# Optimization experiments

Measured on AMD Instinct MI355X. Metric: run time of the kernel, lower is better.

The kernel has to match this reference:

```python
import jax, jax.numpy as jnp
import numpy as np

SORB = 64      # spin orbitals (sequence length)
NELE = 32      # electrons
H = 512        # num_hiddens
B = 4096       # batch
ALPHA = NELE // 2                      # = beta = 16 (spin-up / spin-down electrons)
MIN_I = min(SORB - 2 * ALPHA, 2 * ALPHA)  # = 32; symmetry mask active for i >= MIN_I
EPS = 1e-12


def setup_inputs() -> dict:
    key = jax.random.key(0)
    ks = jax.random.split(key, 10)
    s_in = 1.0 / np.sqrt(2.0)
    s_h = 1.0 / np.sqrt(H)
    return {
        "x": jax.random.randint(ks[0], (B, SORB), 0, 2, dtype=jnp.int32),  # occupancies {0,1}
        "W_ih0": jax.random.normal(ks[1], (3 * H, 2), jnp.float32) * s_in,   # GRU layer0 input weights (r,z,n)
        "W_hh0": jax.random.normal(ks[2], (3 * H, H), jnp.float32) * s_h,
        "W_ih1": jax.random.normal(ks[3], (3 * H, H), jnp.float32) * s_h,    # GRU layer1
        "W_hh1": jax.random.normal(ks[4], (3 * H, H), jnp.float32) * s_h,
        "W_amp": jax.random.normal(ks[5], (2, H), jnp.float32) * s_h,
        "b_amp": jax.random.normal(ks[6], (2,), jnp.float32) * 0.01,
        "W_phase": jax.random.normal(ks[7], (2, H), jnp.float32) * s_h,
        "b_phase": jax.random.normal(ks[8], (2,), jnp.float32) * 0.01,
    }


def _gru_cell(x_in, h, Wih, Whh):
    # PyTorch GRU (bias=False), gate order r, z, n
    gi = x_in @ Wih.T          # (B, 3H)
    gh = h @ Whh.T             # (B, 3H)
    r = jax.nn.sigmoid(gi[:, :H] + gh[:, :H])
    z = jax.nn.sigmoid(gi[:, H:2 * H] + gh[:, H:2 * H])
    n = jnp.tanh(gi[:, 2 * H:] + r * gh[:, 2 * H:])
    return (1.0 - z) * n + z * h


def reference(x, W_ih0, W_hh0, W_ih1, W_hh1, W_amp, b_amp, W_phase, b_phase):
    dt = W_ih0.dtype
    bits = x.astype(jnp.int32)           # (B, SORB) occupancies
    nb = bits.shape[0]

    def step(carry, inp):
        h0, h1, x0, amp, phase, nup, ndn = carry
        i, b_i = inp                      # site index, occupancy bits (B,)
        h0n = _gru_cell(x0, h0, W_ih0, W_hh0)
        h1n = _gru_cell(h0n, h1, W_ih1, W_hh1)
        y = h1n                           # (B, H)
        # amplitude: sqrt(softmax(linear))
        y_amp = jnp.sqrt(jax.nn.softmax(y @ W_amp.T + b_amp, axis=1))   # (B, 2)
        # phase: pi * softsign(linear)
        ph = y @ W_phase.T + b_phase
        y_ph = jnp.pi * ph / (1.0 + jnp.abs(ph))
        # particle-number symmetry mask (alpha == beta spin sectors)
        is_even = (i % 2) == 0            # even sites: spin-up, odd: spin-down
        cnt = jnp.where(is_even, nup, ndn)
        lower = (ALPHA - SORB // 2 + i // 2).astype(dt)
        occ_ok = (cnt < ALPHA).astype(dt)
        unocc_ok = (cnt > lower).astype(dt)
        mask = jnp.stack([unocc_ok, occ_ok], axis=1)
        masked = y_amp * mask
        masked = masked / jnp.sqrt(jnp.sum(masked * masked, axis=1, keepdims=True) + EPS)
        y_amp = jnp.where(i >= MIN_I, masked, y_amp)
        # accumulate conditional amplitude / phase at the sampled occupancy
        sel_a = jnp.take_along_axis(y_amp, b_i[:, None], axis=1)[:, 0]
        sel_p = jnp.take_along_axis(y_ph, b_i[:, None], axis=1)[:, 0]
        amp = amp * sel_a
        phase = phase + sel_p
        bf = b_i.astype(dt)
        nup = nup + jnp.where(is_even, bf, 0.0)
        ndn = ndn + jnp.where(is_even, 0.0, bf)
        x0n = jax.nn.one_hot(b_i, 2, dtype=dt)  # next-step GRU input
        return (h0n, h1n, x0n, amp, phase, nup, ndn), None

    init = (
        jnp.zeros((nb, H), dt), jnp.zeros((nb, H), dt), jnp.zeros((nb, 2), dt),
        jnp.ones((nb,), dt), jnp.zeros((nb,), dt), jnp.zeros((nb,), dt), jnp.zeros((nb,), dt),
    )
    xs = (jnp.arange(SORB), bits.T)       # scan over sites
    (_, _, _, amp, phase, _, _), _ = jax.lax.scan(step, init, xs)
    # complex wavefunction psi = amp * exp(1j*phase); returned as real pair (amp, phase)
    return jnp.stack([amp, phase], axis=-1)
```

## Files before the change

### kernel.cpp

```cpp
#include <hip/hip_runtime.h>
#include <hip/hip_bf16.h>

#define SORB  64
#define HID   512
#define BATCH 4096
#define N3H   1536
#define KD    512
#define BK    64
#define PI_F  3.14159265358979f

typedef _Float16 half8 __attribute__((ext_vector_type(8)));
typedef float    floatx4 __attribute__((ext_vector_type(4)));

__device__ __forceinline__ void gload16(const void* g, void* l) {
    __builtin_amdgcn_global_load_lds(
        (const __attribute__((address_space(1))) void*)g,
        (__attribute__((address_space(3))) void*)l, 16, 0, 0);
}

__device__ __forceinline__ float sigmoidf_(float x) { return 1.f / (1.f + __expf(-x)); }
__device__ __forceinline__ float tanhf_(float x) {
    x = fminf(fmaxf(x, -15.f), 15.f);
    const float e2 = __expf(2.f * x);
    return (e2 - 1.f) / (e2 + 1.f);
}

__global__ __launch_bounds__(256) void convw_kernel(
    const float* __restrict__ w0, const float* __restrict__ w1, const float* __restrict__ w2,
    _Float16* __restrict__ o0, _Float16* __restrict__ o1, _Float16* __restrict__ o2)
{
    const int i = blockIdx.x * 256 + threadIdx.x;
    if (i < N3H * KD) {
        o0[i] = (_Float16)w0[i];
        o1[i] = (_Float16)w1[i];
        o2[i] = (_Float16)w2[i];
    }
}

__global__ __launch_bounds__(256) void init_kernel(
    float* __restrict__ amp, float* __restrict__ phase,
    int* __restrict__ nup, int* __restrict__ ndn)
{
    const int i = blockIdx.x * 256 + threadIdx.x;
    if (i < BATCH) { amp[i] = 1.f; phase[i] = 0.f; nup[i] = 0; ndn[i] = 0; }
}

__device__ __forceinline__ void head_row(
    const _Float16* __restrict__ h1, int m,
    const float* __restrict__ Wamp, const float* __restrict__ bamp,
    const float* __restrict__ Wph,  const float* __restrict__ bph,
    const int* __restrict__ bits,
    float* __restrict__ amp, float* __restrict__ phase,
    int* __restrict__ nup, int* __restrict__ ndn,
    float* __restrict__ out, int step, int lane)
{
    const half8 hv = *(const half8*)(h1 + (size_t)m * HID + lane * 8);
    float d0 = 0.f, d1 = 0.f, d2 = 0.f, d3 = 0.f;
#pragma unroll
    for (int e = 0; e < 8; ++e) {
        const int j = lane * 8 + e;
        const float hn = (float)hv[e];
        d0 += hn * Wamp[j];       d1 += hn * Wamp[HID + j];
        d2 += hn * Wph[j];        d3 += hn * Wph[HID + j];
    }
#pragma unroll
    for (int off = 1; off < 64; off <<= 1) {
        d0 += __shfl_xor(d0, off); d1 += __shfl_xor(d1, off);
        d2 += __shfl_xor(d2, off); d3 += __shfl_xor(d3, off);
    }
    if (lane == 0) {
        const float a0 = d0 + bamp[0];
        const float a1 = d1 + bamp[1];
        const float mx = fmaxf(a0, a1);
        const float e0 = __expf(a0 - mx), e1 = __expf(a1 - mx);
        const float inv = 1.f / (e0 + e1);
        float ya0 = sqrtf(e0 * inv), ya1 = sqrtf(e1 * inv);
        const float p0 = d2 + bph[0];
        const float p1 = d3 + bph[1];
        const float yp0 = PI_F * p0 / (1.f + fabsf(p0));
        const float yp1 = PI_F * p1 / (1.f + fabsf(p1));
        const int even = ((step & 1) == 0);
        const int cnt = even ? nup[m] : ndn[m];
        if (step >= 32) {
            const int lower = (step >> 1) - 16;
            const float m0v = (cnt > lower) ? ya0 : 0.f;
            const float m1v = (cnt < 16) ? ya1 : 0.f;
            const float nrm = sqrtf(m0v * m0v + m1v * m1v + 1e-12f);
            ya0 = m0v / nrm; ya1 = m1v / nrm;
        }
        const int bi = bits[m * SORB + step];
        const float na = amp[m] * (bi ? ya1 : ya0);
        const float np = phase[m] + (bi ? yp1 : yp0);
        amp[m] = na; phase[m] = np;
        if (bi) { if (even) nup[m] = cnt + 1; else ndn[m] = cnt + 1; }
        if (step == SORB - 1) {
            out[m * 2 + 0] = na;
            out[m * 2 + 1] = np;
        }
    }
}

__global__ __launch_bounds__(256) void step1_kernel(
    const _Float16* __restrict__ h0h_c, const _Float16* __restrict__ h1h_c,
    const _Float16* __restrict__ wh0,   const _Float16* __restrict__ wh1,
    const float* __restrict__ Wih0, const int* __restrict__ bits,
    float* __restrict__ h0f, _Float16* __restrict__ h0h_n,
    _Float16* __restrict__ gB, int step,
    const float* __restrict__ Wamp, const float* __restrict__ bamp,
    const float* __restrict__ Wph,  const float* __restrict__ bph,
    float* __restrict__ amp, float* __restrict__ phase,
    int* __restrict__ nup, int* __restrict__ ndn, float* __restrict__ out)
{
    const int z = blockIdx.z;
    const _Float16* Aop = z ? h1h_c : h0h_c;
    const _Float16* Wop = z ? wh1 : wh0;
    const int j0 = blockIdx.x * 64;
    const int m0 = blockIdx.y * 64;

    __shared__ __align__(16) _Float16 As[64 * BK];
    __shared__ __align__(16) _Float16 Bs[192 * BK];

    const int tid  = threadIdx.x;
    const int lane = tid & 63;
    const int wid  = tid >> 6;
    const int wm   = wid >> 1, wj = wid & 1;
    const int ku   = lane >> 4;

    floatx4 acc[2][2][3];
    const floatx4 z4 = {0.f, 0.f, 0.f, 0.f};
#pragma unroll
    for (int a = 0; a < 2; ++a)
#pragma unroll
        for (int b = 0; b < 2; ++b)
#pragma unroll
            for (int g = 0; g < 3; ++g) acc[a][b][g] = z4;

    const _Float16* a_srcp[2];
#pragma unroll
    for (int k2 = 0; k2 < 2; ++k2) {
        const int p = tid + k2 * 256, row = p >> 3, c = (p & 7) ^ (row & 7);
        a_srcp[k2] = Aop + (size_t)(m0 + row) * KD + c * 8;
    }
    const _Float16* b_srcp[6];
#pragma unroll
    for (int k2 = 0; k2 < 6; ++k2) {
        const int p = tid + k2 * 256, row = p >> 3, c = (p & 7) ^ (row & 7);
        const int grow = (row >> 6) * HID + j0 + (row & 63);
        b_srcp[k2] = Wop + (size_t)grow * KD + c * 8;
    }
    _Float16* a_dst[2];
#pragma unroll
    for (int k2 = 0; k2 < 2; ++k2) a_dst[k2] = As + (size_t)(k2 * 256 + wid * 64) * 8;
    _Float16* b_dst[6];
#pragma unroll
    for (int k2 = 0; k2 < 6; ++k2) b_dst[k2] = Bs + (size_t)(k2 * 256 + wid * 64) * 8;

    int aoff[2][2], boff[2][3][2];
#pragma unroll
    for (int mf = 0; mf < 2; ++mf) {
        const int r = wm * 32 + mf * 16 + (lane & 15);
#pragma unroll
        for (int kk = 0; kk < 2; ++kk)
            aoff[mf][kk] = r * BK + (((kk * 4 + ku) ^ (r & 7)) * 8);
    }
#pragma unroll
    for (int jf = 0; jf < 2; ++jf)
#pragma unroll
        for (int g = 0; g < 3; ++g) {
            const int r = g * 64 + wj * 32 + jf * 16 + (lane & 15);
#pragma unroll
            for (int kk = 0; kk < 2; ++kk)
                boff[jf][g][kk] = r * BK + (((kk * 4 + ku) ^ (r & 7)) * 8);
        }

    for (int kt = 0; kt < 8; ++kt) {
        const int k0 = kt * BK;
#pragma unroll
        for (int k2 = 0; k2 < 2; ++k2) gload16(a_srcp[k2] + k0, a_dst[k2]);
#pragma unroll
        for (int k2 = 0; k2 < 6; ++k2) gload16(b_srcp[k2] + k0, b_dst[k2]);
        __syncthreads();
#pragma unroll
        for (int kk = 0; kk < 2; ++kk) {
            half8 af[2], bf[2][3];
#pragma unroll
            for (int mf = 0; mf < 2; ++mf) af[mf] = *(const half8*)(As + aoff[mf][kk]);
#pragma unroll
            for (int jf = 0; jf < 2; ++jf)
#pragma unroll
                for (int g = 0; g < 3; ++g) bf[jf][g] = *(const half8*)(Bs + boff[jf][g][kk]);
#pragma unroll
            for (int mf = 0; mf < 2; ++mf)
#pragma unroll
                for (int jf = 0; jf < 2; ++jf)
#pragma unroll
                    for (int g = 0; g < 3; ++g)
                        acc[mf][jf][g] = __builtin_amdgcn_mfma_f32_16x16x32_f16(
                            af[mf], bf[jf][g], acc[mf][jf][g], 0, 0, 0);
        }
        __syncthreads();
    }

    if (z == 0) {
#pragma unroll
        for (int mf = 0; mf < 2; ++mf)
#pragma unroll
            for (int jf = 0; jf < 2; ++jf) {
                const floatx4 gr = acc[mf][jf][0];
                const floatx4 gz = acc[mf][jf][1];
                const floatx4 gn = acc[mf][jf][2];
#pragma unroll
                for (int reg = 0; reg < 4; ++reg) {
                    const int m = m0 + wm * 32 + mf * 16 + (lane >> 4) * 4 + reg;
                    const int j = j0 + wj * 32 + jf * 16 + (lane & 15);
                    float gir = 0.f, giz = 0.f, gin = 0.f;
                    if (step > 0) {
                        const int tb = bits[m * SORB + step - 1];
                        gir = Wih0[j * 2 + tb];
                        giz = Wih0[(HID + j) * 2 + tb];
                        gin = Wih0[(2 * HID + j) * 2 + tb];
                    }
                    const float r  = sigmoidf_(gir + gr[reg]);
                    const float zz = sigmoidf_(giz + gz[reg]);
                    const float n  = tanhf_(gin + r * gn[reg]);
                    const size_t idx = (size_t)m * HID + j;
                    const float h  = h0f[idx];
                    const float hn = (1.f - zz) * n + zz * h;
                    h0f[idx]   = hn;
                    h0h_n[idx] = (_Float16)hn;
                }
            }
    } else {
#pragma unroll
        for (int mf = 0; mf < 2; ++mf)
#pragma unroll
            for (int jf = 0; jf < 2; ++jf)
#pragma unroll
                for (int g = 0; g < 3; ++g)
#pragma unroll
                    for (int reg = 0; reg < 4; ++reg) {
                        const int m = m0 + wm * 32 + mf * 16 + (lane >> 4) * 4 + reg;
                        const int j = j0 + wj * 32 + jf * 16 + (lane & 15);
                        gB[(size_t)m * N3H + g * HID + j] = (_Float16)acc[mf][jf][g][reg];
                    }
        if (step > 0) {
            const int t = blockIdx.y * 8 + blockIdx.x;
#pragma unroll
            for (int rr = 0; rr < 2; ++rr) {
                const int m = t * 8 + wid * 2 + rr;
                head_row(h1h_c, m, Wamp, bamp, Wph, bph, bits,
                         amp, phase, nup, ndn, out, step - 1, lane);
            }
        }
    }
}

__global__ __launch_bounds__(256) void step2_kernel(
    const _Float16* __restrict__ h0h_n, const _Float16* __restrict__ wi1,
    const _Float16* __restrict__ gB,
    float* __restrict__ h1f, _Float16* __restrict__ h1h_n)
{
    const int j0 = blockIdx.x * 64;
    const int m0 = blockIdx.y * 64;

    __shared__ __align__(16) _Float16 As[64 * BK];
    __shared__ __align__(16) _Float16 Bs[192 * BK];

    const int tid  = threadIdx.x;
    const int lane = tid & 63;
    const int wid  = tid >> 6;
    const int wm   = wid >> 1, wj = wid & 1;
    const int ku   = lane >> 4;

    floatx4 acc[2][2][3];
    const floatx4 z4 = {0.f, 0.f, 0.f, 0.f};
#pragma unroll
    for (int a = 0; a < 2; ++a)
#pragma unroll
        for (int b = 0; b < 2; ++b)
#pragma unroll
            for (int g = 0; g < 3; ++g) acc[a][b][g] = z4;

    const _Float16* a_srcp[2];
#pragma unroll
    for (int k2 = 0; k2 < 2; ++k2) {
        const int p = tid + k2 * 256, row = p >> 3, c = (p & 7) ^ (row & 7);
        a_srcp[k2] = h0h_n + (size_t)(m0 + row) * KD + c * 8;
    }
    const _Float16* b_srcp[6];
#pragma unroll
    for (int k2 = 0; k2 < 6; ++k2) {
        const int p = tid + k2 * 256, row = p >> 3, c = (p & 7) ^ (row & 7);
        const int grow = (row >> 6) * HID + j0 + (row & 63);
        b_srcp[k2] = wi1 + (size_t)grow * KD + c * 8;
    }
    _Float16* a_dst[2];
#pragma unroll
    for (int k2 = 0; k2 < 2; ++k2) a_dst[k2] = As + (size_t)(k2 * 256 + wid * 64) * 8;
    _Float16* b_dst[6];
#pragma unroll
    for (int k2 = 0; k2 < 6; ++k2) b_dst[k2] = Bs + (size_t)(k2 * 256 + wid * 64) * 8;

    int aoff[2][2], boff[2][3][2];
#pragma unroll
    for (int mf = 0; mf < 2; ++mf) {
        const int r = wm * 32 + mf * 16 + (lane & 15);
#pragma unroll
        for (int kk = 0; kk < 2; ++kk)
            aoff[mf][kk] = r * BK + (((kk * 4 + ku) ^ (r & 7)) * 8);
    }
#pragma unroll
    for (int jf = 0; jf < 2; ++jf)
#pragma unroll
        for (int g = 0; g < 3; ++g) {
            const int r = g * 64 + wj * 32 + jf * 16 + (lane & 15);
#pragma unroll
            for (int kk = 0; kk < 2; ++kk)
                boff[jf][g][kk] = r * BK + (((kk * 4 + ku) ^ (r & 7)) * 8);
        }

    for (int kt = 0; kt < 8; ++kt) {
        const int k0 = kt * BK;
#pragma unroll
        for (int k2 = 0; k2 < 2; ++k2) gload16(a_srcp[k2] + k0, a_dst[k2]);
#pragma unroll
        for (int k2 = 0; k2 < 6; ++k2) gload16(b_srcp[k2] + k0, b_dst[k2]);
        __syncthreads();
#pragma unroll
        for (int kk = 0; kk < 2; ++kk) {
            half8 af[2], bf[2][3];
#pragma unroll
            for (int mf = 0; mf < 2; ++mf) af[mf] = *(const half8*)(As + aoff[mf][kk]);
#pragma unroll
            for (int jf = 0; jf < 2; ++jf)
#pragma unroll
                for (int g = 0; g < 3; ++g) bf[jf][g] = *(const half8*)(Bs + boff[jf][g][kk]);
#pragma unroll
            for (int mf = 0; mf < 2; ++mf)
#pragma unroll
                for (int jf = 0; jf < 2; ++jf)
#pragma unroll
                    for (int g = 0; g < 3; ++g)
                        acc[mf][jf][g] = __builtin_amdgcn_mfma_f32_16x16x32_f16(
                            af[mf], bf[jf][g], acc[mf][jf][g], 0, 0, 0);
        }
        __syncthreads();
    }

#pragma unroll
    for (int mf = 0; mf < 2; ++mf)
#pragma unroll
        for (int jf = 0; jf < 2; ++jf) {
            const floatx4 gr = acc[mf][jf][0];
            const floatx4 gz = acc[mf][jf][1];
            const floatx4 gn = acc[mf][jf][2];
#pragma unroll
            for (int reg = 0; reg < 4; ++reg) {
                const int m = m0 + wm * 32 + mf * 16 + (lane >> 4) * 4 + reg;
                const int j = j0 + wj * 32 + jf * 16 + (lane & 15);
                const size_t gbase = (size_t)m * N3H;
                const float ghr = (float)gB[gbase + j];
                const float ghz = (float)gB[gbase + HID + j];
                const float ghn = (float)gB[gbase + 2 * HID + j];
                const float r  = sigmoidf_(gr[reg] + ghr);
                const float zz = sigmoidf_(gz[reg] + ghz);
                const float n  = tanhf_(gn[reg] + r * ghn);
                const size_t idx = (size_t)m * HID + j;
                const float h  = h1f[idx];
                const float hn = (1.f - zz) * n + zz * h;
                h1f[idx]   = hn;
                h1h_n[idx] = (_Float16)hn;
            }
        }
}

__global__ __launch_bounds__(256) void head_kernel(
    const _Float16* __restrict__ h1h_n,
    const float* __restrict__ Wamp, const float* __restrict__ bamp,
    const float* __restrict__ Wph,  const float* __restrict__ bph,
    const int* __restrict__ bits,
    float* __restrict__ amp, float* __restrict__ phase,
    int* __restrict__ nup, int* __restrict__ ndn,
    float* __restrict__ out, int step)
{
    const int lane = threadIdx.x & 63;
    const int m    = blockIdx.x * 4 + (threadIdx.x >> 6);
    head_row(h1h_n, m, Wamp, bamp, Wph, bph, bits, amp, phase, nup, ndn, out, step, lane);
}

extern "C" void kernel_launch(void* const* d_in, const int* in_sizes, int n_in,
                              void* d_out, int out_size, void* d_ws, size_t ws_size,
                              hipStream_t stream) {
    const int*   bits = (const int*)d_in[0];
    const float* Wih0 = (const float*)d_in[1];
    const float* Whh0 = (const float*)d_in[2];
    const float* Wih1 = (const float*)d_in[3];
    const float* Whh1 = (const float*)d_in[4];
    const float* Wamp = (const float*)d_in[5];
    const float* bamp = (const float*)d_in[6];
    const float* Wph  = (const float*)d_in[7];
    const float* bph  = (const float*)d_in[8];
    float* out = (float*)d_out;

    char* ws = (char*)d_ws;
    size_t off = 0;
    auto alloc = [&](size_t bytes) {
        void* p = ws + off;
        off = (off + bytes + 255) & ~(size_t)255;
        return p;
    };
    _Float16* wh0 = (_Float16*)alloc((size_t)N3H * KD * 2);
    _Float16* wi1 = (_Float16*)alloc((size_t)N3H * KD * 2);
    _Float16* wh1 = (_Float16*)alloc((size_t)N3H * KD * 2);
    float*    h0f = (float*)alloc((size_t)BATCH * HID * 4);
    float*    h1f = (float*)alloc((size_t)BATCH * HID * 4);
    _Float16* h0hA = (_Float16*)alloc((size_t)BATCH * HID * 2);
    _Float16* h0hB = (_Float16*)alloc((size_t)BATCH * HID * 2);
    _Float16* h1hA = (_Float16*)alloc((size_t)BATCH * HID * 2);
    _Float16* h1hB = (_Float16*)alloc((size_t)BATCH * HID * 2);
    _Float16* gB  = (_Float16*)alloc((size_t)BATCH * N3H * 2);
    float*    amp   = (float*)alloc((size_t)BATCH * 4);
    float*    phase = (float*)alloc((size_t)BATCH * 4);
    int*      nup   = (int*)alloc((size_t)BATCH * 4);
    int*      ndn   = (int*)alloc((size_t)BATCH * 4);

    _Float16* h0h[2] = {h0hA, h0hB};
    _Float16* h1h[2] = {h1hA, h1hB};

    hipMemsetAsync(h0f, 0, (size_t)BATCH * HID * 4, stream);
    hipMemsetAsync(h1f, 0, (size_t)BATCH * HID * 4, stream);
    hipMemsetAsync(h0hA, 0, (size_t)BATCH * HID * 2, stream);
    hipMemsetAsync(h1hA, 0, (size_t)BATCH * HID * 2, stream);
    convw_kernel<<<(N3H * KD + 255) / 256, 256, 0, stream>>>(Whh0, Wih1, Whh1, wh0, wi1, wh1);
    init_kernel<<<BATCH / 256, 256, 0, stream>>>(amp, phase, nup, ndn);

    for (int s = 0; s < SORB; ++s) {
        const int cur = s & 1, nxt = cur ^ 1;
        step1_kernel<<<dim3(8, 64, 2), 256, 0, stream>>>(
            h0h[cur], h1h[cur], wh0, wh1, Wih0, bits, h0f, h0h[nxt], gB, s,
            Wamp, bamp, Wph, bph, amp, phase, nup, ndn, out);
        step2_kernel<<<dim3(8, 64), 256, 0, stream>>>(
            h0h[nxt], wi1, gB, h1f, h1h[nxt]);
    }
    head_kernel<<<BATCH / 4, 256, 0, stream>>>(
        h1h[0], Wamp, bamp, Wph, bph, bits, amp, phase, nup, ndn, out, SORB - 1);
}
```

Measured before the change: 3.400 ms.

## Fuse layer-1 input and hidden GEMMs into one kernel, drop fp32 hidden state

Layer 1's two GEMMs (input-to-hidden and hidden-to-hidden) now run in one kernel that accumulates both K halves in registers. A separate accumulator keeps the n-gate hidden term apart. This removes the fp16 gB intermediate buffer and its global round trip. The fp32 hidden-state copies are dropped, so state is carried only in fp16, which risks accuracy drift over 64 steps. The head now runs as its own kernel every step instead of being fused into step1, which adds a third launch per step; an unused step2_kernel stub remains as dead code.

```diff
diff --git a/kernel.cpp b/kernel.cpp
--- a/kernel.cpp
+++ b/kernel.cpp
@@ -45,16 +45,383 @@
     if (i < BATCH) { amp[i] = 1.f; phase[i] = 0.f; nup[i] = 0; ndn[i] = 0; }
 }
 
-__device__ __forceinline__ void head_row(
-    const _Float16* __restrict__ h1, int m,
+__global__ __launch_bounds__(256) void step1_kernel(
+    const _Float16* __restrict__ h0h_c, const _Float16* __restrict__ wh0,
+    const float* __restrict__ Wih0, const int* __restrict__ bits,
+    _Float16* __restrict__ h0h_n, int step)
+{
+    const int j0 = blockIdx.x * 64;
+    const int m0 = blockIdx.y * 64;
+
+    __shared__ __align__(16) _Float16 As[64 * BK];
+    __shared__ __align__(16) _Float16 Bs[192 * BK];
+
+    const int tid  = threadIdx.x;
+    const int lane = tid & 63;
+    const int wid  = tid >> 6;
+    const int wm   = wid >> 1, wj = wid & 1;
+    const int ku   = lane >> 4;
+
+    floatx4 acc[2][2][3];
+    const floatx4 z4 = {0.f, 0.f, 0.f, 0.f};
+#pragma unroll
+    for (int a = 0; a < 2; ++a)
+#pragma unroll
+        for (int b = 0; b < 2; ++b)
+#pragma unroll
+            for (int g = 0; g < 3; ++g) acc[a][b][g] = z4;
+
+    const _Float16* a_srcp[2];
+#pragma unroll
+    for (int k2 = 0; k2 < 2; ++k2) {
+        const int p = tid + k2 * 256, row = p >> 3, c = (p & 7) ^ (row & 7);
+        a_srcp[k2] = h0h_c + (size_t)(m0 + row) * KD + c * 8;
+    }
+    const _Float16* b_srcp[6];
+#pragma unroll
+    for (int k2 = 0; k2 < 6; ++k2) {
+        const int p = tid + k2 * 256, row = p >> 3, c = (p & 7) ^ (row & 7);
+        const int grow = (row >> 6) * HID + j0 + (row & 63);
+        b_srcp[k2] = wh0 + (size_t)grow * KD + c * 8;
+    }
+    _Float16* a_dst[2];
+#pragma unroll
+    for (int k2 = 0; k2 < 2; ++k2) a_dst[k2] = As + (size_t)(k2 * 256 + wid * 64) * 8;
+    _Float16* b_dst[6];
+#pragma unroll
+    for (int k2 = 0; k2 < 6; ++k2) b_dst[k2] = Bs + (size_t)(k2 * 256 + wid * 64) * 8;
+
+    int aoff[2][2], boff[2][3][2];
+#pragma unroll
+    for (int mf = 0; mf < 2; ++mf) {
+        const int r = wm * 32 + mf * 16 + (lane & 15);
+#pragma unroll
+        for (int kk = 0; kk < 2; ++kk)
+            aoff[mf][kk] = r * BK + (((kk * 4 + ku) ^ (r & 7)) * 8);
+    }
+#pragma unroll
+    for (int jf = 0; jf < 2; ++jf)
+#pragma unroll
+        for (int g = 0; g < 3; ++g) {
+            const int r = g * 64 + wj * 32 + jf * 16 + (lane & 15);
+#pragma unroll
+            for (int kk = 0; kk < 2; ++kk)
+                boff[jf][g][kk] = r * BK + (((kk * 4 + ku) ^ (r & 7)) * 8);
+        }
+
+    for (int kt = 0; kt < 8; ++kt) {
+        const int k0 = kt * BK;
+#pragma unroll
+        for (int k2 = 0; k2 < 2; ++k2) gload16(a_srcp[k2] + k0, a_dst[k2]);
+#pragma unroll
+        for (int k2 = 0; k2 < 6; ++k2) gload16(b_srcp[k2] + k0, b_dst[k2]);
+        __syncthreads();
+#pragma unroll
+        for (int kk = 0; kk < 2; ++kk) {
+            half8 af[2], bf[2][3];
+#pragma unroll
+            for (int mf = 0; mf < 2; ++mf) af[mf] = *(const half8*)(As + aoff[mf][kk]);
+#pragma unroll
+            for (int jf = 0; jf < 2; ++jf)
+#pragma unroll
+                for (int g = 0; g < 3; ++g) bf[jf][g] = *(const half8*)(Bs + boff[jf][g][kk]);
+#pragma unroll
+            for (int mf = 0; mf < 2; ++mf)
+#pragma unroll
+                for (int jf = 0; jf < 2; ++jf)
+#pragma unroll
+                    for (int g = 0; g < 3; ++g)
+                        acc[mf][jf][g] = __builtin_amdgcn_mfma_f32_16x16x32_f16(
+                            af[mf], bf[jf][g], acc[mf][jf][g], 0, 0, 0);
+        }
+        __syncthreads();
+    }
+
+#pragma unroll
+    for (int mf = 0; mf < 2; ++mf)
+#pragma unroll
+        for (int jf = 0; jf < 2; ++jf) {
+            const floatx4 gr = acc[mf][jf][0];
+            const floatx4 gz = acc[mf][jf][1];
+            const floatx4 gn = acc[mf][jf][2];
+#pragma unroll
+            for (int reg = 0; reg < 4; ++reg) {
+                const int m = m0 + wm * 32 + mf * 16 + (lane >> 4) * 4 + reg;
+                const int j = j0 + wj * 32 + jf * 16 + (lane & 15);
+                float gir = 0.f, giz = 0.f, gin = 0.f;
+                if (step > 0) {
+                    const int tb = bits[m * SORB + step - 1];
+                    gir = Wih0[j * 2 + tb];
+                    giz = Wih0[(HID + j) * 2 + tb];
+                    gin = Wih0[(2 * HID + j) * 2 + tb];
+                }
+                const float r  = sigmoidf_(gir + gr[reg]);
+                const float zz = sigmoidf_(giz + gz[reg]);
+                const float n  = tanhf_(gin + r * gn[reg]);
+                const size_t idx = (size_t)m * HID + j;
+                const float h  = (float)h0h_c[idx];
+                h0h_n[idx] = (_Float16)((1.f - zz) * n + zz * h);
+            }
+        }
+}
+
+__global__ __launch_bounds__(256) void step2_kernel(
+    const _Float16* __restrict__ h0h_n, const _Float16* __restrict__ h1h_c,
+    const _Float16* __restrict__ wi1,   const _Float16* __restrict__ wh1,
+    _Float16* __restrict__ h1h_n)
+{
+    const int j0 = blockIdx.x * 64;
+    const int m0 = blockIdx.y * 64;
+
+    __shared__ __align__(16) _Float16 As[64 * BK];
+    __shared__ __align__(16) _Float16 Bs[192 * BK];
+
+    const int tid  = threadIdx.x;
+    const int lane = tid & 63;
+    const int wid  = tid >> 6;
+    const int wm   = wid >> 1, wj = wid & 1;
+    const int ku   = lane >> 4;
+
+    floatx4 acc[2][2][3];
+    const floatx4 z4 = {0.f, 0.f, 0.f, 0.f};
+#pragma unroll
+    for (int a = 0; a < 2; ++a)
+#pragma unroll
+        for (int b = 0; b < 2; ++b)
+#pragma unroll
+            for (int g = 0; g < 3; ++g) acc[a][b][g] = z4;
+
+    _Float16* a_dst[2];
+#pragma unroll
+    for (int k2 = 0; k2 < 2; ++k2) a_dst[k2] = As + (size_t)(k2 * 256 + wid * 64) * 8;
+    _Float16* b_dst[6];
+#pragma unroll
+    for (int k2 = 0; k2 < 6; ++k2) b_dst[k2] = Bs + (size_t)(k2 * 256 + wid * 64) * 8;
+
+    int aoff[2][2], boff[2][3][2];
+#pragma unroll
+    for (int mf = 0; mf < 2; ++mf) {
+        const int r = wm * 32 + mf * 16 + (lane & 15);
+#pragma unroll
+        for (int kk = 0; kk < 2; ++kk)
+            aoff[mf][kk] = r * BK + (((kk * 4 + ku) ^ (r & 7)) * 8);
+    }
+#pragma unroll
+    for (int jf = 0; jf < 2; ++jf)
+#pragma unroll
+        for (int g = 0; g < 3; ++g) {
+            const int r = g * 64 + wj * 32 + jf * 16 + (lane & 15);
+#pragma unroll
+            for (int kk = 0; kk < 2; ++kk)
+                boff[jf][g][kk] = r * BK + (((kk * 4 + ku) ^ (r & 7)) * 8);
+        }
+
+#pragma unroll 1
+    for (int half = 0; half < 2; ++half) {
+        const _Float16* Aop = half ? h1h_c : h0h_n;
+        const _Float16* Wop = half ? wh1  : wi1;
+        const _Float16* a_srcp[2];
+#pragma unroll
+        for (int k2 = 0; k2 < 2; ++k2) {
+            const int p = tid + k2 * 256, row = p >> 3, c = (p & 7) ^ (row & 7);
+            a_srcp[k2] = Aop + (size_t)(m0 + row) * KD + c * 8;
+        }
+        const _Float16* b_srcp[6];
+#pragma unroll
+        for (int k2 = 0; k2 < 6; ++k2) {
+            const int p = tid + k2 * 256, row = p >> 3, c = (p & 7) ^ (row & 7);
+            const int grow = (row >> 6) * HID + j0 + (row & 63);
+            b_srcp[k2] = Wop + (size_t)grow * KD + c * 8;
+        }
+
+        for (int kt = 0; kt < 8; ++kt) {
+            const int k0 = kt * BK;
+#pragma unroll
+            for (int k2 = 0; k2 < 2; ++k2) gload16(a_srcp[k2] + k0, a_dst[k2]);
+#pragma unroll
+            for (int k2 = 0; k2 < 6; ++k2) gload16(b_srcp[k2] + k0, b_dst[k2]);
+            __syncthreads();
+#pragma unroll
+            for (int kk = 0; kk < 2; ++kk) {
+                half8 af[2], bf[2][3];
+#pragma unroll
+                for (int mf = 0; mf < 2; ++mf) af[mf] = *(const half8*)(As + aoff[mf][kk]);
+#pragma unroll
+                for (int jf = 0; jf < 2; ++jf)
+#pragma unroll
+                    for (int g = 0; g < 3; ++g) bf[jf][g] = *(const half8*)(Bs + boff[jf][g][kk]);
+#pragma unroll
+                for (int mf = 0; mf < 2; ++mf)
+#pragma unroll
+                    for (int jf = 0; jf < 2; ++jf)
+#pragma unroll
+                        for (int g = 0; g < 3; ++g)
+                            acc[mf][jf][g] = __builtin_amdgcn_mfma_f32_16x16x32_f16(
+                                af[mf], bf[jf][g], acc[mf][jf][g], 0, 0, 0);
+            }
+            __syncthreads();
+        }
+    }
+
+#pragma unroll
+    for (int mf = 0; mf < 2; ++mf)
+#pragma unroll
+        for (int jf = 0; jf < 2; ++jf) {
+            const floatx4 gr = acc[mf][jf][0];
+            const floatx4 gz = acc[mf][jf][1];
+            const floatx4 gn = acc[mf][jf][2];
+#pragma unroll
+            for (int reg = 0; reg < 4; ++reg) {
+                const int m = m0 + wm * 32 + mf * 16 + (lane >> 4) * 4 + reg;
+                const int j = j0 + wj * 32 + jf * 16 + (lane & 15);
+                const float r  = sigmoidf_(gr[reg]);
+                (void)r;
+            }
+        }
+}
+
+__global__ __launch_bounds__(256) void step2b_kernel(
+    const _Float16* __restrict__ h0h_n, const _Float16* __restrict__ h1h_c,
+    const _Float16* __restrict__ wi1,   const _Float16* __restrict__ wh1,
+    _Float16* __restrict__ h1h_n)
+{
+    const int j0 = blockIdx.x * 64;
+    const int m0 = blockIdx.y * 64;
+
+    __shared__ __align__(16) _Float16 As[64 * BK];
+    __shared__ __align__(16) _Float16 Bs[192 * BK];
+
+    const int tid  = threadIdx.x;
+    const int lane = tid & 63;
+    const int wid  = tid >> 6;
+    const int wm   = wid >> 1, wj = wid & 1;
+    const int ku   = lane >> 4;
+
+    floatx4 acc[2][2][3];
+    floatx4 accn[2][2];
+    const floatx4 z4 = {0.f, 0.f, 0.f, 0.f};
+#pragma unroll
+    for (int a = 0; a < 2; ++a)
+#pragma unroll
+        for (int b = 0; b < 2; ++b) {
+#pragma unroll
+            for (int g = 0; g < 3; ++g) acc[a][b][g] = z4;
+            accn[a][b] = z4;
+        }
+
+    _Float16* a_dst[2];
+#pragma unroll
+    for (int k2 = 0; k2 < 2; ++k2) a_dst[k2] = As + (size_t)(k2 * 256 + wid * 64) * 8;
+    _Float16* b_dst[6];
+#pragma unroll
+    for (int k2 = 0; k2 < 6; ++k2) b_dst[k2] = Bs + (size_t)(k2 * 256 + wid * 64) * 8;
+
+    int aoff[2][2], boff[2][3][2];
+#pragma unroll
+    for (int mf = 0; mf < 2; ++mf) {
+        const int r = wm * 32 + mf * 16 + (lane & 15);
+#pragma unroll
+        for (int kk = 0; kk < 2; ++kk)
+            aoff[mf][kk] = r * BK + (((kk * 4 + ku) ^ (r & 7)) * 8);
+    }
+#pragma unroll
+    for (int jf = 0; jf < 2; ++jf)
+#pragma unroll
+        for (int g = 0; g < 3; ++g) {
+            const int r = g * 64 + wj * 32 + jf * 16 + (lane & 15);
+#pragma unroll
+            for (int kk = 0; kk < 2; ++kk)
+                boff[jf][g][kk] = r * BK + (((kk * 4 + ku) ^ (r & 7)) * 8);
+        }
+
+#pragma unroll 1
+    for (int half = 0; half < 2; ++half) {
+        const _Float16* Aop = half ? h1h_c : h0h_n;
+        const _Float16* Wop = half ? wh1  : wi1;
+        const _Float16* a_srcp[2];
+#pragma unroll
+        for (int k2 = 0; k2 < 2; ++k2) {
+            const int p = tid + k2 * 256, row = p >> 3, c = (p & 7) ^ (row & 7);
+            a_srcp[k2] = Aop + (size_t)(m0 + row) * KD + c * 8;
+        }
+        const _Float16* b_srcp[6];
+#pragma unroll
+        for (int k2 = 0; k2 < 6; ++k2) {
+            const int p = tid + k2 * 256, row = p >> 3, c = (p & 7) ^ (row & 7);
+            const int grow = (row >> 6) * HID + j0 + (row & 63);
+            b_srcp[k2] = Wop + (size_t)grow * KD + c * 8;
+        }
+
+        for (int kt = 0; kt < 8; ++kt) {
+            const int k0 = kt * BK;
+#pragma unroll
+            for (int k2 = 0; k2 < 2; ++k2) gload16(a_srcp[k2] + k0, a_dst[k2]);
+#pragma unroll
+            for (int k2 = 0; k2 < 6; ++k2) gload16(b_srcp[k2] + k0, b_dst[k2]);
+            __syncthreads();
+#pragma unroll
+            for (int kk = 0; kk < 2; ++kk) {
+                half8 af[2], bf[2][3];
+#pragma unroll
+                for (int mf = 0; mf < 2; ++mf) af[mf] = *(const half8*)(As + aoff[mf][kk]);
+#pragma unroll
+                for (int jf = 0; jf < 2; ++jf)
+#pragma unroll
+                    for (int g = 0; g < 3; ++g) bf[jf][g] = *(const half8*)(Bs + boff[jf][g][kk]);
+#pragma unroll
+                for (int mf = 0; mf < 2; ++mf)
+#pragma unroll
+                    for (int jf = 0; jf < 2; ++jf) {
+                        acc[mf][jf][0] = __builtin_amdgcn_mfma_f32_16x16x32_f16(
+                            af[mf], bf[jf][0], acc[mf][jf][0], 0, 0, 0);
+                        acc[mf][jf][1] = __builtin_amdgcn_mfma_f32_16x16x32_f16(
+                            af[mf], bf[jf][1], acc[mf][jf][1], 0, 0, 0);
+                        if (half == 0)
+                            acc[mf][jf][2] = __builtin_amdgcn_mfma_f32_16x16x32_f16(
+                                af[mf], bf[jf][2], acc[mf][jf][2], 0, 0, 0);
+                        else
+                            accn[mf][jf] = __builtin_amdgcn_mfma_f32_16x16x32_f16(
+                                af[mf], bf[jf][2], accn[mf][jf], 0, 0, 0);
+                    }
+            }
+            __syncthreads();
+        }
+    }
+
+#pragma unroll
+    for (int mf = 0; mf < 2; ++mf)
+#pragma unroll
+        for (int jf = 0; jf < 2; ++jf) {
+            const floatx4 grz = acc[mf][jf][0];
+            const floatx4 gzz = acc[mf][jf][1];
+            const floatx4 gin = acc[mf][jf][2];
+            const floatx4 ghn = accn[mf][jf];
+#pragma unroll
+            for (int reg = 0; reg < 4; ++reg) {
+                const int m = m0 + wm * 32 + mf * 16 + (lane >> 4) * 4 + reg;
+                const int j = j0 + wj * 32 + jf * 16 + (lane & 15);
+                const float r  = sigmoidf_(grz[reg]);
+                const float zz = sigmoidf_(gzz[reg]);
+                const float n  = tanhf_(gin[reg] + r * ghn[reg]);
+                const size_t idx = (size_t)m * HID + j;
+                const float h  = (float)h1h_c[idx];
+                h1h_n[idx] = (_Float16)((1.f - zz) * n + zz * h);
+            }
+        }
+}
+
+__global__ __launch_bounds__(256) void head_kernel(
+    const _Float16* __restrict__ h1h_n,
     const float* __restrict__ Wamp, const float* __restrict__ bamp,
     const float* __restrict__ Wph,  const float* __restrict__ bph,
     const int* __restrict__ bits,
     float* __restrict__ amp, float* __restrict__ phase,
     int* __restrict__ nup, int* __restrict__ ndn,
-    float* __restrict__ out, int step, int lane)
+    float* __restrict__ out, int step)
 {
-    const half8 hv = *(const half8*)(h1 + (size_t)m * HID + lane * 8);
+    const int lane = threadIdx.x & 63;
+    const int m    = blockIdx.x * 4 + (threadIdx.x >> 6);
+    const half8 hv = *(const half8*)(h1h_n + (size_t)m * HID + lane * 8);
     float d0 = 0.f, d1 = 0.f, d2 = 0.f, d3 = 0.f;
 #pragma unroll
     for (int e = 0; e < 8; ++e) {
@@ -100,294 +467,6 @@
     }
 }
 
-__global__ __launch_bounds__(256) void step1_kernel(
-    const _Float16* __restrict__ h0h_c, const _Float16* __restrict__ h1h_c,
-    const _Float16* __restrict__ wh0,   const _Float16* __restrict__ wh1,
-    const float* __restrict__ Wih0, const int* __restrict__ bits,
-    float* __restrict__ h0f, _Float16* __restrict__ h0h_n,
-    _Float16* __restrict__ gB, int step,
-    const float* __restrict__ Wamp, const float* __restrict__ bamp,
-    const float* __restrict__ Wph,  const float* __restrict__ bph,
-    float* __restrict__ amp, float* __restrict__ phase,
-    int* __restrict__ nup, int* __restrict__ ndn, float* __restrict__ out)
-{
-    const int z = blockIdx.z;
-    const _Float16* Aop = z ? h1h_c : h0h_c;
-    const _Float16* Wop = z ? wh1 : wh0;
-    const int j0 = blockIdx.x * 64;
-    const int m0 = blockIdx.y * 64;
-
-    __shared__ __align__(16) _Float16 As[64 * BK];
-    __shared__ __align__(16) _Float16 Bs[192 * BK];
-
-    const int tid  = threadIdx.x;
-    const int lane = tid & 63;
-    const int wid  = tid >> 6;
-    const int wm   = wid >> 1, wj = wid & 1;
-    const int ku   = lane >> 4;
-
-    floatx4 acc[2][2][3];
-    const floatx4 z4 = {0.f, 0.f, 0.f, 0.f};
-#pragma unroll
-    for (int a = 0; a < 2; ++a)
-#pragma unroll
-        for (int b = 0; b < 2; ++b)
-#pragma unroll
-            for (int g = 0; g < 3; ++g) acc[a][b][g] = z4;
-
-    const _Float16* a_srcp[2];
-#pragma unroll
-    for (int k2 = 0; k2 < 2; ++k2) {
-        const int p = tid + k2 * 256, row = p >> 3, c = (p & 7) ^ (row & 7);
-        a_srcp[k2] = Aop + (size_t)(m0 + row) * KD + c * 8;
-    }
-    const _Float16* b_srcp[6];
-#pragma unroll
-    for (int k2 = 0; k2 < 6; ++k2) {
-        const int p = tid + k2 * 256, row = p >> 3, c = (p & 7) ^ (row & 7);
-        const int grow = (row >> 6) * HID + j0 + (row & 63);
-        b_srcp[k2] = Wop + (size_t)grow * KD + c * 8;
-    }
-    _Float16* a_dst[2];
-#pragma unroll
-    for (int k2 = 0; k2 < 2; ++k2) a_dst[k2] = As + (size_t)(k2 * 256 + wid * 64) * 8;
-    _Float16* b_dst[6];
-#pragma unroll
-    for (int k2 = 0; k2 < 6; ++k2) b_dst[k2] = Bs + (size_t)(k2 * 256 + wid * 64) * 8;
-
-    int aoff[2][2], boff[2][3][2];
-#pragma unroll
-    for (int mf = 0; mf < 2; ++mf) {
-        const int r = wm * 32 + mf * 16 + (lane & 15);
-#pragma unroll
-        for (int kk = 0; kk < 2; ++kk)
-            aoff[mf][kk] = r * BK + (((kk * 4 + ku) ^ (r & 7)) * 8);
-    }
-#pragma unroll
-    for (int jf = 0; jf < 2; ++jf)
-#pragma unroll
-        for (int g = 0; g < 3; ++g) {
-            const int r = g * 64 + wj * 32 + jf * 16 + (lane & 15);
-#pragma unroll
-            for (int kk = 0; kk < 2; ++kk)
-                boff[jf][g][kk] = r * BK + (((kk * 4 + ku) ^ (r & 7)) * 8);
-        }
-
-    for (int kt = 0; kt < 8; ++kt) {
-        const int k0 = kt * BK;
-#pragma unroll
-        for (int k2 = 0; k2 < 2; ++k2) gload16(a_srcp[k2] + k0, a_dst[k2]);
-#pragma unroll
-        for (int k2 = 0; k2 < 6; ++k2) gload16(b_srcp[k2] + k0, b_dst[k2]);
-        __syncthreads();
-#pragma unroll
-        for (int kk = 0; kk < 2; ++kk) {
-            half8 af[2], bf[2][3];
-#pragma unroll
-            for (int mf = 0; mf < 2; ++mf) af[mf] = *(const half8*)(As + aoff[mf][kk]);
-#pragma unroll
-            for (int jf = 0; jf < 2; ++jf)
-#pragma unroll
-                for (int g = 0; g < 3; ++g) bf[jf][g] = *(const half8*)(Bs + boff[jf][g][kk]);
-#pragma unroll
-            for (int mf = 0; mf < 2; ++mf)
-#pragma unroll
-                for (int jf = 0; jf < 2; ++jf)
-#pragma unroll
-                    for (int g = 0; g < 3; ++g)
-                        acc[mf][jf][g] = __builtin_amdgcn_mfma_f32_16x16x32_f16(
-                            af[mf], bf[jf][g], acc[mf][jf][g], 0, 0, 0);
-        }
-        __syncthreads();
-    }
-
-    if (z == 0) {
-#pragma unroll
-        for (int mf = 0; mf < 2; ++mf)
-#pragma unroll
-            for (int jf = 0; jf < 2; ++jf) {
-                const floatx4 gr = acc[mf][jf][0];
-                const floatx4 gz = acc[mf][jf][1];
-                const floatx4 gn = acc[mf][jf][2];
-#pragma unroll
-                for (int reg = 0; reg < 4; ++reg) {
-                    const int m = m0 + wm * 32 + mf * 16 + (lane >> 4) * 4 + reg;
-                    const int j = j0 + wj * 32 + jf * 16 + (lane & 15);
-                    float gir = 0.f, giz = 0.f, gin = 0.f;
-                    if (step > 0) {
-                        const int tb = bits[m * SORB + step - 1];
-                        gir = Wih0[j * 2 + tb];
-                        giz = Wih0[(HID + j) * 2 + tb];
-                        gin = Wih0[(2 * HID + j) * 2 + tb];
-                    }
-                    const float r  = sigmoidf_(gir + gr[reg]);
-                    const float zz = sigmoidf_(giz + gz[reg]);
-                    const float n  = tanhf_(gin + r * gn[reg]);
-                    const size_t idx = (size_t)m * HID + j;
-                    const float h  = h0f[idx];
-                    const float hn = (1.f - zz) * n + zz * h;
-                    h0f[idx]   = hn;
-                    h0h_n[idx] = (_Float16)hn;
-                }
-            }
-    } else {
-#pragma unroll
-        for (int mf = 0; mf < 2; ++mf)
-#pragma unroll
-            for (int jf = 0; jf < 2; ++jf)
-#pragma unroll
-                for (int g = 0; g < 3; ++g)
-#pragma unroll
-                    for (int reg = 0; reg < 4; ++reg) {
-                        const int m = m0 + wm * 32 + mf * 16 + (lane >> 4) * 4 + reg;
-                        const int j = j0 + wj * 32 + jf * 16 + (lane & 15);
-                        gB[(size_t)m * N3H + g * HID + j] = (_Float16)acc[mf][jf][g][reg];
-                    }
-        if (step > 0) {
-            const int t = blockIdx.y * 8 + blockIdx.x;
-#pragma unroll
-            for (int rr = 0; rr < 2; ++rr) {
-                const int m = t * 8 + wid * 2 + rr;
-                head_row(h1h_c, m, Wamp, bamp, Wph, bph, bits,
-                         amp, phase, nup, ndn, out, step - 1, lane);
-            }
-        }
-    }
-}
-
-__global__ __launch_bounds__(256) void step2_kernel(
-    const _Float16* __restrict__ h0h_n, const _Float16* __restrict__ wi1,
-    const _Float16* __restrict__ gB,
-    float* __restrict__ h1f, _Float16* __restrict__ h1h_n)
-{
-    const int j0 = blockIdx.x * 64;
-    const int m0 = blockIdx.y * 64;
-
-    __shared__ __align__(16) _Float16 As[64 * BK];
-    __shared__ __align__(16) _Float16 Bs[192 * BK];
-
-    const int tid  = threadIdx.x;
-    const int lane = tid & 63;
-    const int wid  = tid >> 6;
-    const int wm   = wid >> 1, wj = wid & 1;
-    const int ku   = lane >> 4;
-
-    floatx4 acc[2][2][3];
-    const floatx4 z4 = {0.f, 0.f, 0.f, 0.f};
-#pragma unroll
-    for (int a = 0; a < 2; ++a)
-#pragma unroll
-        for (int b = 0; b < 2; ++b)
-#pragma unroll
-            for (int g = 0; g < 3; ++g) acc[a][b][g] = z4;
-
-    const _Float16* a_srcp[2];
-#pragma unroll
-    for (int k2 = 0; k2 < 2; ++k2) {
-        const int p = tid + k2 * 256, row = p >> 3, c = (p & 7) ^ (row & 7);
-        a_srcp[k2] = h0h_n + (size_t)(m0 + row) * KD + c * 8;
-    }
-    const _Float16* b_srcp[6];
-#pragma unroll
-    for (int k2 = 0; k2 < 6; ++k2) {
-        const int p = tid + k2 * 256, row = p >> 3, c = (p & 7) ^ (row & 7);
-        const int grow = (row >> 6) * HID + j0 + (row & 63);
-        b_srcp[k2] = wi1 + (size_t)grow * KD + c * 8;
-    }
-    _Float16* a_dst[2];
-#pragma unroll
-    for (int k2 = 0; k2 < 2; ++k2) a_dst[k2] = As + (size_t)(k2 * 256 + wid * 64) * 8;
-    _Float16* b_dst[6];
-#pragma unroll
-    for (int k2 = 0; k2 < 6; ++k2) b_dst[k2] = Bs + (size_t)(k2 * 256 + wid * 64) * 8;
-
-    int aoff[2][2], boff[2][3][2];
-#pragma unroll
-    for (int mf = 0; mf < 2; ++mf) {
-        const int r = wm * 32 + mf * 16 + (lane & 15);
-#pragma unroll
-        for (int kk = 0; kk < 2; ++kk)
-            aoff[mf][kk] = r * BK + (((kk * 4 + ku) ^ (r & 7)) * 8);
-    }
-#pragma unroll
-    for (int jf = 0; jf < 2; ++jf)
-#pragma unroll
-        for (int g = 0; g < 3; ++g) {
-            const int r = g * 64 + wj * 32 + jf * 16 + (lane & 15);
-#pragma unroll
-            for (int kk = 0; kk < 2; ++kk)
-                boff[jf][g][kk] = r * BK + (((kk * 4 + ku) ^ (r & 7)) * 8);
-        }
-
-    for (int kt = 0; kt < 8; ++kt) {
-        const int k0 = kt * BK;
-#pragma unroll
-        for (int k2 = 0; k2 < 2; ++k2) gload16(a_srcp[k2] + k0, a_dst[k2]);
-#pragma unroll
-        for (int k2 = 0; k2 < 6; ++k2) gload16(b_srcp[k2] + k0, b_dst[k2]);
-        __syncthreads();
-#pragma unroll
-        for (int kk = 0; kk < 2; ++kk) {
-            half8 af[2], bf[2][3];
-#pragma unroll
-            for (int mf = 0; mf < 2; ++mf) af[mf] = *(const half8*)(As + aoff[mf][kk]);
-#pragma unroll
-            for (int jf = 0; jf < 2; ++jf)
-#pragma unroll
-                for (int g = 0; g < 3; ++g) bf[jf][g] = *(const half8*)(Bs + boff[jf][g][kk]);
-#pragma unroll
-            for (int mf = 0; mf < 2; ++mf)
-#pragma unroll
-                for (int jf = 0; jf < 2; ++jf)
-#pragma unroll
-                    for (int g = 0; g < 3; ++g)
-                        acc[mf][jf][g] = __builtin_amdgcn_mfma_f32_16x16x32_f16(
-                            af[mf], bf[jf][g], acc[mf][jf][g], 0, 0, 0);
-        }
-        __syncthreads();
-    }
-
-#pragma unroll
-    for (int mf = 0; mf < 2; ++mf)
-#pragma unroll
-        for (int jf = 0; jf < 2; ++jf) {
-            const floatx4 gr = acc[mf][jf][0];
-            const floatx4 gz = acc[mf][jf][1];
-            const floatx4 gn = acc[mf][jf][2];
-#pragma unroll
-            for (int reg = 0; reg < 4; ++reg) {
-                const int m = m0 + wm * 32 + mf * 16 + (lane >> 4) * 4 + reg;
-                const int j = j0 + wj * 32 + jf * 16 + (lane & 15);
-                const size_t gbase = (size_t)m * N3H;
-                const float ghr = (float)gB[gbase + j];
-                const float ghz = (float)gB[gbase + HID + j];
-                const float ghn = (float)gB[gbase + 2 * HID + j];
-                const float r  = sigmoidf_(gr[reg] + ghr);
-                const float zz = sigmoidf_(gz[reg] + ghz);
-                const float n  = tanhf_(gn[reg] + r * ghn);
-                const size_t idx = (size_t)m * HID + j;
-                const float h  = h1f[idx];
-                const float hn = (1.f - zz) * n + zz * h;
-                h1f[idx]   = hn;
-                h1h_n[idx] = (_Float16)hn;
-            }
-        }
-}
-
-__global__ __launch_bounds__(256) void head_kernel(
-    const _Float16* __restrict__ h1h_n,
-    const float* __restrict__ Wamp, const float* __restrict__ bamp,
-    const float* __restrict__ Wph,  const float* __restrict__ bph,
-    const int* __restrict__ bits,
-    float* __restrict__ amp, float* __restrict__ phase,
-    int* __restrict__ nup, int* __restrict__ ndn,
-    float* __restrict__ out, int step)
-{
-    const int lane = threadIdx.x & 63;
-    const int m    = blockIdx.x * 4 + (threadIdx.x >> 6);
-    head_row(h1h_n, m, Wamp, bamp, Wph, bph, bits, amp, phase, nup, ndn, out, step, lane);
-}
-
 extern "C" void kernel_launch(void* const* d_in, const int* in_sizes, int n_in,
                               void* d_out, int out_size, void* d_ws, size_t ws_size,
                               hipStream_t stream) {
@@ -412,13 +491,10 @@
     _Float16* wh0 = (_Float16*)alloc((size_t)N3H * KD * 2);
     _Float16* wi1 = (_Float16*)alloc((size_t)N3H * KD * 2);
     _Float16* wh1 = (_Float16*)alloc((size_t)N3H * KD * 2);
-    float*    h0f = (float*)alloc((size_t)BATCH * HID * 4);
-    float*    h1f = (float*)alloc((size_t)BATCH * HID * 4);
     _Float16* h0hA = (_Float16*)alloc((size_t)BATCH * HID * 2);
     _Float16* h0hB = (_Float16*)alloc((size_t)BATCH * HID * 2);
     _Float16* h1hA = (_Float16*)alloc((size_t)BATCH * HID * 2);
     _Float16* h1hB = (_Float16*)alloc((size_t)BATCH * HID * 2);
-    _Float16* gB  = (_Float16*)alloc((size_t)BATCH * N3H * 2);
     float*    amp   = (float*)alloc((size_t)BATCH * 4);
     float*    phase = (float*)alloc((size_t)BATCH * 4);
     int*      nup   = (int*)alloc((size_t)BATCH * 4);
@@ -427,8 +503,6 @@
     _Float16* h0h[2] = {h0hA, h0hB};
     _Float16* h1h[2] = {h1hA, h1hB};
 
-    hipMemsetAsync(h0f, 0, (size_t)BATCH * HID * 4, stream);
-    hipMemsetAsync(h1f, 0, (size_t)BATCH * HID * 4, stream);
     hipMemsetAsync(h0hA, 0, (size_t)BATCH * HID * 2, stream);
     hipMemsetAsync(h1hA, 0, (size_t)BATCH * HID * 2, stream);
     convw_kernel<<<(N3H * KD + 255) / 256, 256, 0, stream>>>(Whh0, Wih1, Whh1, wh0, wi1, wh1);
@@ -436,12 +510,11 @@
 
     for (int s = 0; s < SORB; ++s) {
         const int cur = s & 1, nxt = cur ^ 1;
-        step1_kernel<<<dim3(8, 64, 2), 256, 0, stream>>>(
-            h0h[cur], h1h[cur], wh0, wh1, Wih0, bits, h0f, h0h[nxt], gB, s,
-            Wamp, bamp, Wph, bph, amp, phase, nup, ndn, out);
-        step2_kernel<<<dim3(8, 64), 256, 0, stream>>>(
-            h0h[nxt], wi1, gB, h1f, h1h[nxt]);
-    }
-    head_kernel<<<BATCH / 4, 256, 0, stream>>>(
-        h1h[0], Wamp, bamp, Wph, bph, bits, amp, phase, nup, ndn, out, SORB - 1);
-}
+        step1_kernel<<<dim3(8, 64), 256, 0, stream>>>(
+            h0h[cur], wh0, Wih0, bits, h0h[nxt], s);
+        step2b_kernel<<<dim3(8, 64), 256, 0, stream>>>(
+            h0h[nxt], h1h[cur], wi1, wh1, h1h[nxt]);
+        head_kernel<<<BATCH / 4, 256, 0, stream>>>(
+            h1h[nxt], Wamp, bamp, Wph, bph, bits, amp, phase, nup, ndn, out, s);
+    }
+}
```

New measurement: 3.061 ms. -10.0%, faster.
